# Optimization experiments

Hardware: AMD Instinct MI355X
Metric: run time of the kernel (lower is better)

Reference implementation:

```python
import jax, jax.numpy as jnp
import numpy as np
from jax import lax

B, L, E = 16, 100, 128
NQ, NC, DL = 1000, 100, 100
NODE, PATH, MAXC = 5000, 5000, 128


def setup_inputs() -> dict:
    key = jax.random.key(0)
    ks = jax.random.split(key, 40)
    rn = lambda k, *s: jax.random.normal(k, s, jnp.float32) * 0.02
    inp = {}
    inp['code'] = jax.random.randint(ks[0], (B, L, NQ * 2 + MAXC * 3), 0, NODE, jnp.int32)
    inp['q'] = jax.random.randint(ks[1], (B, L), 0, NQ, jnp.int32)
    inp['c'] = jax.random.randint(ks[2], (B, L), 0, NC, jnp.int32)
    inp['sd'] = jax.random.randint(ks[3], (B, L), 0, DL, jnp.int32)
    inp['qd'] = jax.random.randint(ks[4], (B, L), 0, DL, jnp.int32)
    inp['a'] = jax.random.randint(ks[5], (B, L), 0, NQ * 2, jnp.int32)
    inp['qshft'] = jax.random.randint(ks[6], (B, L), 0, NQ, jnp.int32)
    inp['cshft'] = jax.random.randint(ks[7], (B, L), 0, NC, jnp.int32)
    inp['sdshft'] = jax.random.randint(ks[8], (B, L), 0, DL, jnp.int32)
    inp['qdshft'] = jax.random.randint(ks[9], (B, L), 0, DL, jnp.int32)
    # embedding tables (padding rows zeroed, matching torch padding_idx)
    inp['embed_nodes'] = rn(ks[10], NODE + 2, E)
    inp['embed_paths'] = rn(ks[11], PATH + 2, E)
    inp['q_tab'] = rn(ks[12], NQ + 1, E).at[NQ].set(0.0)
    inp['c_tab'] = rn(ks[13], NC + 1, E).at[NC].set(0.0)
    inp['sd_tab'] = rn(ks[14], DL + 100, E).at[0].set(0.0)
    inp['qd_tab'] = rn(ks[15], DL + 100, E).at[0].set(0.0)
    inp['a_tab'] = rn(ks[16], NQ * 2 + 2, E).at[2].set(0.0)
    inp['knowledge'] = rn(ks[17], 1, E)
    # linear weights stored [in, out] so y = x @ W + b
    inp['Wpt'] = rn(ks[18], 3 * E, 3 * E); inp['bpt'] = rn(ks[19], 3 * E)
    inp['Wat'] = rn(ks[20], 3 * E, 1);     inp['bat'] = rn(ks[21], 1)
    inp['Wqa'] = rn(ks[22], 4 * E, E);     inp['bqa'] = rn(ks[23], E)
    inp['W1'] = rn(ks[24], 4 * E, E);      inp['b1'] = rn(ks[25], E)
    inp['W2'] = rn(ks[26], E, E);          inp['b2'] = rn(ks[27], E)
    inp['W3'] = rn(ks[28], E, E);          inp['b3'] = rn(ks[29], E)
    inp['W4'] = rn(ks[30], 2 * E, E);      inp['b4'] = rn(ks[31], E)
    inp['W5'] = rn(ks[32], 2 * E, E);      inp['b5'] = rn(ks[33], E)
    inp['W6'] = rn(ks[34], 4 * E, E);      inp['b6'] = rn(ks[35], E)
    inp['Wf'] = rn(ks[36], E, 10);         inp['bf'] = rn(ks[37], 10)
    return inp


def reference(code, q, c, sd, qd, a, qshft, cshft, sdshft, qdshft,
              embed_nodes, embed_paths, q_tab, c_tab, sd_tab, qd_tab, a_tab,
              knowledge, Wpt, bpt, Wat, bat, Wqa, bqa, W1, b1, W2, b2, W3, b3,
              W4, b4, W5, b5, W6, b6, Wf, bf):
    Bq, Lq = q.shape
    # ---- code2vec attention over AST paths ----
    c2v = code[:, :, NQ * 2:].reshape(Bq, Lq, MAXC, 3)
    full = jnp.concatenate([embed_nodes[c2v[..., 0]],
                            embed_nodes[c2v[..., 2]],
                            embed_paths[c2v[..., 1]]], axis=-1)  # [B,L,MAXC,3E]
    tr = jnp.tanh(full @ Wpt + bpt)
    ctx = tr @ Wat + bat                      # [B,L,MAXC,1]
    attn = jax.nn.softmax(ctx, axis=1)        # softmax over seq dim (dim=1), as in source
    code_vec = jnp.sum(full * attn, axis=2)   # [B,L,3E]
    # ---- embeddings + input projections ----
    a_e = a_tab[a]
    acode = jnp.concatenate([a_e, code_vec], axis=-1) @ Wqa + bqa   # [B,L,E]
    inp = jnp.concatenate([q_tab[q], c_tab[c], sd_tab[sd], qd_tab[qd]], axis=-1) @ W1 + b1
    sd_e = sd_tab[sd]
    qd_e = qd_tab[qd]
    # ---- sequential SDF/PKA/KSU recurrence ----
    k0 = jnp.tile(knowledge, (Bq, 1))  # [B,E]

    def step(k, ts):
        inp_t, a_t, sd_t, qd_t = ts
        qq = inp_t - k
        sdf = jax.nn.sigmoid(qq @ W2 + b2) * jnp.tanh(qq @ W3 + b3)
        x = jnp.concatenate([sdf, a_t], axis=-1)
        pka = jax.nn.sigmoid(x @ W4 + b4) * jnp.tanh(x @ W5 + b5)
        ins = jnp.concatenate([k, a_t, sd_t, qd_t], axis=-1)
        g = jax.nn.sigmoid(ins @ W6 + b6)
        k_new = g * k + (1.0 - g) * pka
        return k_new, k_new @ Wf + bf

    xs = (inp.transpose(1, 0, 2), acode.transpose(1, 0, 2),
          sd_e.transpose(1, 0, 2), qd_e.transpose(1, 0, 2))
    _, logits = lax.scan(step, k0, xs)        # [L,B,10]
    return jax.nn.sigmoid(logits.transpose(1, 0, 2))  # [B,L,10]
```

## Files before the change

### kernel.cpp

```cpp
#include <hip/hip_runtime.h>
#include <hip/hip_bf16.h>

#define B_   16
#define L_   100
#define E_   128
#define NQ_  1000
#define MAXC_ 128
#define CODE_STRIDE (NQ_*2 + MAXC_*3)
#define CODE_OFF    (NQ_*2)

typedef short bf16x8 __attribute__((ext_vector_type(8)));
typedef float f32x4  __attribute__((ext_vector_type(4)));

__device__ __forceinline__ unsigned short f2b(float f) {
    unsigned u = __float_as_uint(f);
    unsigned r = (u + 0x7fffu + ((u >> 16) & 1u)) >> 16;
    return (unsigned short)r;
}
__device__ __forceinline__ unsigned cvt2(float lo, float hi) {
    unsigned r;
    asm("v_cvt_pk_bf16_f32 %0, %1, %2" : "=v"(r) : "v"(lo), "v"(hi));
    return r;
}
__device__ __forceinline__ float fsig(float x) {
    return __builtin_amdgcn_rcpf(1.0f + __builtin_amdgcn_exp2f(-1.44269504f * x));
}
__device__ __forceinline__ float ftanh(float x) {
    return 1.0f - 2.0f * __builtin_amdgcn_rcpf(1.0f + __builtin_amdgcn_exp2f(2.88539008f * x));
}
__device__ __forceinline__ void ldsbar() {
    asm volatile("s_waitcnt lgkmcnt(0)" ::: "memory");
    __builtin_amdgcn_s_barrier();
}
__device__ __forceinline__ void vmbar() {
    asm volatile("s_waitcnt vmcnt(0) lgkmcnt(0)" ::: "memory");
    __builtin_amdgcn_s_barrier();
}
__device__ __forceinline__ void gll16(const void* g, void* l) {
    __builtin_amdgcn_global_load_lds(
        (const __attribute__((address_space(1))) unsigned int*)g,
        (__attribute__((address_space(3))) unsigned int*)l, 16, 0, 0);
}

#define P0 576
#define P1 (P0+2501)
#define P2 (P1+2501)
#define P3 (P2+192)
#define P4 (P3+128)
#define P5 (P4+8)
#define P6 (P5+512)
#define P7 (P6+256)
#define P8 (P7+192)

__global__ void k_prep(const float* __restrict__ Wpt, const float* __restrict__ en,
                       const float* __restrict__ ep,
                       const float* __restrict__ W2, const float* __restrict__ W3,
                       const float* __restrict__ W4, const float* __restrict__ W5,
                       const float* __restrict__ W6, const float* __restrict__ Wf,
                       const float* __restrict__ Wqa, const float* __restrict__ W1,
                       unsigned short* __restrict__ wptT, unsigned short* __restrict__ enb,
                       unsigned short* __restrict__ epb, unsigned short* __restrict__ bt1,
                       unsigned short* __restrict__ bt2, unsigned short* __restrict__ btf,
                       unsigned short* __restrict__ bW1, unsigned short* __restrict__ bW2,
                       unsigned short* __restrict__ bW6)
{
    int blk = blockIdx.x;
    if (blk < P0) {
        int i = blk * 256 + threadIdx.x;
        if (i < 384*384) {
            int e = i & 7, G = i >> 3;
            int l15g = G & 15, rest = G >> 4;
            int l4g = rest & 3, rest2 = rest >> 2;
            int ksg = rest2 % 12, tile = rest2 / 12;
            int n = tile*16 + l15g, k = ksg*32 + l4g*8 + e;
            wptT[i] = f2b(Wpt[k*384 + n]);
        }
    } else if (blk < P1) {
        int i = (blk - P0) * 256 + threadIdx.x;
        if (i < 5002*128) enb[i] = f2b(en[i]);
    } else if (blk < P2) {
        int i = (blk - P1) * 256 + threadIdx.x;
        if (i < 5002*128) epb[i] = f2b(ep[i]);
    } else if (blk < P3) {
        int i = (blk - P2) * 256 + threadIdx.x;
        int n = i >> 7, k = i & 127;
        float v = (n < 128) ? W2[k*128 + n] : (n < 256) ? W3[k*128 + (n-128)]
                                                        : W6[k*128 + (n-256)];
        bt1[i] = f2b(v);
    } else if (blk < P4) {
        int i = (blk - P3) * 256 + threadIdx.x;
        int n = i >> 7, k = i & 127;
        float v = (n < 128) ? W4[k*128 + n] : W5[k*128 + (n-128)];
        bt2[i] = f2b(v);
    } else if (blk < P5) {
        int i = (blk - P4) * 256 + threadIdx.x;
        int n = i >> 7, k = i & 127;
        btf[i] = f2b(n < 10 ? Wf[k*10 + n] : 0.0f);
    } else if (blk < P6) {
        int i = (blk - P5) * 256 + threadIdx.x;
        int n = i >> 9, k = i & 511;
        float v = (n < 128) ? Wqa[k*128 + n] : W1[k*128 + (n-128)];
        bW1[i] = f2b(v);
    } else if (blk < P7) {
        int i = (blk - P6) * 256 + threadIdx.x;
        int n = i >> 7, k = i & 127;
        float v = (n < 128) ? W2[k*128 + n]
                : (n < 256) ? W3[k*128 + (n-128)]
                : (n < 384) ? W4[(128 + k)*128 + (n-256)]
                            : W5[(128 + k)*128 + (n-384)];
        bW2[i] = f2b(v);
    } else {
        int i = (blk - P7) * 256 + threadIdx.x;
        if (i < 128*384) {
            int n = i / 384, k = i % 384;
            bW6[i] = f2b(W6[(128 + k)*128 + n]);
        }
    }
}

__global__ __launch_bounds__(256, 3) void k_ctx(const int* __restrict__ code,
    const unsigned short* __restrict__ enb, const unsigned short* __restrict__ epb,
    const unsigned short* __restrict__ wptT, const float* __restrict__ bpt,
    const float* __restrict__ wat, const float* __restrict__ bat,
    float* __restrict__ ctx)
{
    __shared__ __align__(16) unsigned short Bs[2][12288];
    __shared__ float bw[768];
    const int tid = threadIdx.x, wv = tid >> 6, lane = tid & 63;
    const int l15 = lane & 15, l4 = lane >> 4;
    const int rowg0 = blockIdx.x * 128;

    for (int idx = tid; idx < 768; idx += 256)
        bw[idx] = (idx < 384) ? bpt[idx] : wat[idx - 384];

    bf16x8 af[2][12];
    #pragma unroll
    for (int h = 0; h < 2; ++h) {
        int rowg = rowg0 + h * 64 + wv * 16 + l15;
        int m = rowg & 127, bl = rowg >> 7;
        const int* cp = code + (size_t)bl * CODE_STRIDE + CODE_OFF + m * 3;
        int i0 = cp[0], i1 = cp[1], i2 = cp[2];
        #pragma unroll
        for (int ks = 0; ks < 12; ++ks) {
            int seg = ks >> 2;
            int idx = (seg == 0) ? i0 : (seg == 1 ? i2 : i1);
            const unsigned short* tab = (seg == 2) ? epb : enb;
            af[h][ks] = *(const bf16x8*)(tab + (size_t)idx * 128 + (ks & 3) * 32 + l4 * 8);
        }
    }

    {
        const unsigned short* src = wptT;
        #pragma unroll
        for (int i = 0; i < 6; ++i) {
            int jj = wv * 6 + i;
            gll16(src + jj * 512 + lane * 8, &Bs[0][jj * 512]);
        }
    }

    float cr[2][4] = {{0.f,0.f,0.f,0.f},{0.f,0.f,0.f,0.f}};
    const float bat0 = bat[0];

    for (int nc = 0; nc < 12; ++nc) {
        vmbar();
        if (nc < 11) {
            const unsigned short* src = wptT + (size_t)(nc + 1) * 12288;
            #pragma unroll
            for (int i = 0; i < 6; ++i) {
                int jj = wv * 6 + i;
                gll16(src + jj * 512 + lane * 8, &Bs[(nc + 1) & 1][jj * 512]);
            }
        }
        const char* bb0 = (const char*)&Bs[nc & 1][0] + l15 * 16;
        const char* bb1 = bb0 + 12288;
        f32x4 acc00 = {0.f,0.f,0.f,0.f}, acc01 = {0.f,0.f,0.f,0.f};
        f32x4 acc10 = {0.f,0.f,0.f,0.f}, acc11 = {0.f,0.f,0.f,0.f};
        #pragma unroll
        for (int ks = 0; ks < 12; ++ks) {
            int go = (ks * 4 + l4) * 256;
            bf16x8 b0 = *(const bf16x8*)(bb0 + go);
            bf16x8 b1 = *(const bf16x8*)(bb1 + go);
            acc00 = __builtin_amdgcn_mfma_f32_16x16x32_bf16(af[0][ks], b0, acc00, 0, 0, 0);
            acc01 = __builtin_amdgcn_mfma_f32_16x16x32_bf16(af[0][ks], b1, acc01, 0, 0, 0);
            acc10 = __builtin_amdgcn_mfma_f32_16x16x32_bf16(af[1][ks], b0, acc10, 0, 0, 0);
            acc11 = __builtin_amdgcn_mfma_f32_16x16x32_bf16(af[1][ks], b1, acc11, 0, 0, 0);
        }
        int ng0 = nc * 32 + l15, ng1 = ng0 + 16;
        float bv0 = bw[ng0], wa0 = bw[384 + ng0];
        float bv1 = bw[ng1], wa1 = bw[384 + ng1];
        #pragma unroll
        for (int r = 0; r < 4; ++r) {
            cr[0][r] += ftanh(acc00[r] + bv0) * wa0 + ftanh(acc01[r] + bv1) * wa1;
            cr[1][r] += ftanh(acc10[r] + bv0) * wa0 + ftanh(acc11[r] + bv1) * wa1;
        }
    }

    #pragma unroll
    for (int h = 0; h < 2; ++h)
        #pragma unroll
        for (int r = 0; r < 4; ++r) {
            float v = cr[h][r];
            v += __shfl_xor(v, 1); v += __shfl_xor(v, 2);
            v += __shfl_xor(v, 4); v += __shfl_xor(v, 8);
            cr[h][r] = v;
        }
    if (l15 == 0) {
        #pragma unroll
        for (int h = 0; h < 2; ++h) {
            int rbase = rowg0 + h * 64 + wv * 16 + l4 * 4;
            #pragma unroll
            for (int r = 0; r < 4; ++r) ctx[rbase + r] = cr[h][r] + bat0;
        }
    }
}

__global__ void k_softmax(const float* __restrict__ ctx, float* __restrict__ attn)
{
    int t = blockIdx.x * 256 + threadIdx.x;
    if (t >= B_ * MAXC_) return;
    int b = t >> 7, m = t & 127;
    const float* p = ctx + (size_t)b * L_ * MAXC_ + m;
    float mx = -1e30f;
    for (int l = 0; l < L_; ++l) mx = fmaxf(mx, p[l * MAXC_]);
    float s = 0.f;
    for (int l = 0; l < L_; ++l) s += __expf(p[l * MAXC_] - mx);
    float inv = 1.0f / s;
    float* o = attn + (size_t)b * L_ * MAXC_ + m;
    for (int l = 0; l < L_; ++l) o[l * MAXC_] = __expf(p[l * MAXC_] - mx) * inv;
}

__global__ __launch_bounds__(192) void k_codevec(const int* __restrict__ code,
    const float* __restrict__ attn, const unsigned short* __restrict__ enb,
    const unsigned short* __restrict__ epb, float* __restrict__ cv)
{
    int bl = blockIdx.x;
    int t = threadIdx.x;
    int seg = t >> 6, tc = t & 63;
    const int* cp = code + (size_t)bl * CODE_STRIDE + CODE_OFF;
    const float* ap = attn + (size_t)bl * MAXC_;
    const unsigned short* tab = (seg == 2) ? epb : enb;
    const int sidx = (seg == 0) ? 0 : (seg == 1) ? 2 : 1;
    float ax = 0.f, ay = 0.f;
    #pragma unroll 8
    for (int m = 0; m < MAXC_; ++m) {
        float w = ap[m];
        int idx = cp[m * 3 + sidx];
        unsigned u = *((const unsigned*)(tab + (size_t)idx * 128) + tc);
        ax += w * __uint_as_float(u << 16);
        ay += w * __uint_as_float(u & 0xffff0000u);
    }
    float2 o; o.x = ax; o.y = ay;
    *(float2*)(cv + (size_t)bl * 384 + seg * 128 + tc * 2) = o;
}

__global__ __launch_bounds__(256) void k_fuse(
    const int* __restrict__ a, const int* __restrict__ q, const int* __restrict__ c,
    const int* __restrict__ sd, const int* __restrict__ qd,
    const float* __restrict__ a_tab, const float* __restrict__ q_tab,
    const float* __restrict__ c_tab, const float* __restrict__ sd_tab,
    const float* __restrict__ qd_tab, const float* __restrict__ cv,
    const unsigned short* __restrict__ bW1, const unsigned short* __restrict__ bW2,
    const unsigned short* __restrict__ bW6,
    const float* __restrict__ bqa, const float* __restrict__ b1,
    const float* __restrict__ b2, const float* __restrict__ b3,
    const float* __restrict__ b4, const float* __restrict__ b5,
    const float* __restrict__ b6,
    float4* __restrict__ preQ, float* __restrict__ pre6)
{
    __shared__ __align__(16) unsigned short X[16 * 1024];
    __shared__ __align__(16) unsigned short Y[16 * 256];
    const int tid = threadIdx.x, wv = tid >> 6, lane = tid & 63;
    const int l15 = lane & 15, l4 = lane >> 4;
    const int row0 = blockIdx.x * 16;

    #pragma unroll
    for (int it = 0; it < 16; ++it) {
        int idx = tid + it * 256;
        int r = idx >> 8, col = (idx & 255) * 4;
        int row = row0 + r;
        const float* src;
        if (col < 128)       src = a_tab + (size_t)a[row] * 128 + col;
        else if (col < 512)  src = cv + (size_t)row * 384 + (col - 128);
        else if (col < 640)  src = q_tab + (size_t)q[row] * 128 + (col - 512);
        else if (col < 768)  src = c_tab + (size_t)c[row] * 128 + (col - 640);
        else if (col < 896)  src = sd_tab + (size_t)sd[row] * 128 + (col - 768);
        else                 src = qd_tab + (size_t)qd[row] * 128 + (col - 896);
        float4 v = *(const float4*)src;
        unsigned u0 = cvt2(v.x, v.y), u1 = cvt2(v.z, v.w);
        int byte = r * 2048 + ((((col >> 3)) ^ (r & 7)) << 4) + ((col & 4) << 1);
        *(unsigned*)((char*)X + byte) = u0;
        *(unsigned*)((char*)X + byte + 4) = u1;
    }
    ldsbar();

    {
        bf16x8 ak[16];
        int kbase = (wv < 2) ? 0 : 512;
        #pragma unroll
        for (int ks = 0; ks < 16; ++ks) {
            int col = kbase + ks * 32 + l4 * 8;
            ak[ks] = *(const bf16x8*)((const char*)X + l15 * 2048 + (((col >> 3) ^ (l15 & 7)) << 4));
        }
        int nbase = wv * 64;
        f32x4 acc[4] = {{0,0,0,0},{0,0,0,0},{0,0,0,0},{0,0,0,0}};
        #pragma unroll
        for (int i = 0; i < 4; ++i) {
            const unsigned short* bp = bW1 + (size_t)(nbase + i * 16 + l15) * 512 + l4 * 8;
            #pragma unroll
            for (int ks = 0; ks < 16; ++ks) {
                bf16x8 bfr = *(const bf16x8*)(bp + ks * 32);
                acc[i] = __builtin_amdgcn_mfma_f32_16x16x32_bf16(ak[ks], bfr, acc[i], 0, 0, 0);
            }
        }
        #pragma unroll
        for (int i = 0; i < 4; ++i) {
            int cc = nbase + i * 16 + l15;
            float bias = (cc < 128) ? bqa[cc] : b1[cc - 128];
            #pragma unroll
            for (int rr = 0; rr < 4; ++rr) {
                int row = l4 * 4 + rr;
                int byte = row * 512 + (((cc >> 3) ^ (row & 7)) << 4) + (cc & 7) * 2;
                *(unsigned short*)((char*)Y + byte) = f2b(acc[i][rr] + bias);
            }
        }
    }
    ldsbar();

    bf16x8 zi[4], za[4], zs[4], zq[4];
    #pragma unroll
    for (int ks = 0; ks < 4; ++ks) {
        int ci = 128 + ks * 32 + l4 * 8;
        zi[ks] = *(const bf16x8*)((const char*)Y + l15 * 512 + (((ci >> 3) ^ (l15 & 7)) << 4));
        int ca = ks * 32 + l4 * 8;
        za[ks] = *(const bf16x8*)((const char*)Y + l15 * 512 + (((ca >> 3) ^ (l15 & 7)) << 4));
        int cs = 768 + ks * 32 + l4 * 8;
        zs[ks] = *(const bf16x8*)((const char*)X + l15 * 2048 + (((cs >> 3) ^ (l15 & 7)) << 4));
        int cq = 896 + ks * 32 + l4 * 8;
        zq[ks] = *(const bf16x8*)((const char*)X + l15 * 2048 + (((cq >> 3) ^ (l15 & 7)) << 4));
    }
    f32x4 A2[2] = {{0,0,0,0},{0,0,0,0}}, A3[2] = {{0,0,0,0},{0,0,0,0}};
    f32x4 A4[2] = {{0,0,0,0},{0,0,0,0}}, A5[2] = {{0,0,0,0},{0,0,0,0}};
    f32x4 A6[2] = {{0,0,0,0},{0,0,0,0}};
    #pragma unroll
    for (int tt = 0; tt < 2; ++tt) {
        int n = wv * 32 + tt * 16 + l15;
        const unsigned short* p2 = bW2 + (size_t)(      n) * 128 + l4 * 8;
        const unsigned short* p3 = bW2 + (size_t)(128 + n) * 128 + l4 * 8;
        const unsigned short* p4 = bW2 + (size_t)(256 + n) * 128 + l4 * 8;
        const unsigned short* p5 = bW2 + (size_t)(384 + n) * 128 + l4 * 8;
        const unsigned short* p6 = bW6 + (size_t)n * 384 + l4 * 8;
        #pragma unroll
        for (int ks = 0; ks < 4; ++ks) {
            A2[tt] = __builtin_amdgcn_mfma_f32_16x16x32_bf16(zi[ks], *(const bf16x8*)(p2 + ks*32), A2[tt], 0, 0, 0);
            A3[tt] = __builtin_amdgcn_mfma_f32_16x16x32_bf16(zi[ks], *(const bf16x8*)(p3 + ks*32), A3[tt], 0, 0, 0);
            A4[tt] = __builtin_amdgcn_mfma_f32_16x16x32_bf16(za[ks], *(const bf16x8*)(p4 + ks*32), A4[tt], 0, 0, 0);
            A5[tt] = __builtin_amdgcn_mfma_f32_16x16x32_bf16(za[ks], *(const bf16x8*)(p5 + ks*32), A5[tt], 0, 0, 0);
            A6[tt] = __builtin_amdgcn_mfma_f32_16x16x32_bf16(za[ks], *(const bf16x8*)(p6 + ks*32), A6[tt], 0, 0, 0);
        }
        #pragma unroll
        for (int ks = 0; ks < 4; ++ks)
            A6[tt] = __builtin_amdgcn_mfma_f32_16x16x32_bf16(zs[ks], *(const bf16x8*)(p6 + 256 + ks*32), A6[tt], 0, 0, 0);
        #pragma unroll
        for (int ks = 0; ks < 4; ++ks)
            A6[tt] = __builtin_amdgcn_mfma_f32_16x16x32_bf16(zq[ks], *(const bf16x8*)(p6 + 512 + ks*32), A6[tt], 0, 0, 0);
    }
    #pragma unroll
    for (int tt = 0; tt < 2; ++tt) {
        int n = wv * 32 + tt * 16 + l15;
        float c2 = b2[n], c3 = b3[n], c4 = b4[n], c5 = b5[n], c6 = b6[n];
        #pragma unroll
        for (int rr = 0; rr < 4; ++rr) {
            size_t row = (size_t)(row0 + l4 * 4 + rr);
            float4 o;
            o.x = A2[tt][rr] + c2; o.y = A3[tt][rr] + c3;
            o.z = A4[tt][rr] + c4; o.w = A5[tt][rr] + c5;
            preQ[row * 128 + n] = o;
            pre6[row * 128 + n] = A6[tt][rr] + c6;
        }
    }
}

__global__ __launch_bounds__(512) void k_recur(
    const unsigned short* __restrict__ bt1, const unsigned short* __restrict__ bt2,
    const float* __restrict__ knowledge, const float4* __restrict__ preQ,
    const float* __restrict__ pre6, unsigned short* __restrict__ khist)
{
    __shared__ __align__(16) unsigned short k_lds[16 * 128];
    __shared__ __align__(16) unsigned short s_lds[16 * 128];
    const int tid = threadIdx.x, wv = tid >> 6, lane = tid & 63;
    const int l15 = lane & 15, l4 = lane >> 4;
    const int j = wv * 16 + l15;

    bf16x8 w2f[4], w3f[4], w6f[4], w4f[4], w5f[4];
    #pragma unroll
    for (int ks = 0; ks < 4; ++ks) {
        w2f[ks] = *(const bf16x8*)(bt1 + (size_t)(      j) * 128 + ks * 32 + l4 * 8);
        w3f[ks] = *(const bf16x8*)(bt1 + (size_t)(128 + j) * 128 + ks * 32 + l4 * 8);
        w6f[ks] = *(const bf16x8*)(bt1 + (size_t)(256 + j) * 128 + ks * 32 + l4 * 8);
        w4f[ks] = *(const bf16x8*)(bt2 + (size_t)(      j) * 128 + ks * 32 + l4 * 8);
        w5f[ks] = *(const bf16x8*)(bt2 + (size_t)(128 + j) * 128 + ks * 32 + l4 * 8);
    }

    float kreg[4], gR[4];
    {
        float k0 = knowledge[j];
        unsigned short kb = f2b(k0);
        #pragma unroll
        for (int r = 0; r < 4; ++r) {
            kreg[r] = k0;
            int b = l4 * 4 + r;
            k_lds[b * 128 + (((j >> 3) ^ b) << 3) + (j & 7)] = kb;
        }
    }
    ldsbar();

    float4 pv[4]; float p6[4];
    #pragma unroll
    for (int r = 0; r < 4; ++r) {
        int b = l4 * 4 + r;
        size_t ix = (size_t)(b * L_) * 128 + j;
        pv[r] = preQ[ix]; p6[r] = pre6[ix];
    }

    for (int t = 0; t < L_; ++t) {
        float4 pvN[4]; float p6N[4];
        #pragma unroll
        for (int r = 0; r < 4; ++r) {
            int b = l4 * 4 + r;
            size_t ix = (size_t)(b * L_ + t + 1) * 128 + j;
            pvN[r] = preQ[ix]; p6N[r] = pre6[ix];
        }

        bf16x8 ak[4];
        {
            const unsigned short* kb = k_lds + l15 * 128;
            #pragma unroll
            for (int ks = 0; ks < 4; ++ks)
                ak[ks] = *(const bf16x8*)(kb + (((ks * 4 + l4) ^ l15) << 3));
        }
        f32x4 a2 = {0,0,0,0}, a3 = {0,0,0,0}, a6 = {0,0,0,0};
        #pragma unroll
        for (int ks = 0; ks < 4; ++ks) {
            a2 = __builtin_amdgcn_mfma_f32_16x16x32_bf16(ak[ks], w2f[ks], a2, 0, 0, 0);
            a3 = __builtin_amdgcn_mfma_f32_16x16x32_bf16(ak[ks], w3f[ks], a3, 0, 0, 0);
            a6 = __builtin_amdgcn_mfma_f32_16x16x32_bf16(ak[ks], w6f[ks], a6, 0, 0, 0);
        }
        #pragma unroll
        for (int r = 0; r < 4; ++r) {
            int b = l4 * 4 + r;
            float sdf = fsig(pv[r].x - a2[r]) * ftanh(pv[r].y - a3[r]);
            gR[r] = fsig(a6[r] + p6[r]);
            s_lds[b * 128 + (((j >> 3) ^ b) << 3) + (j & 7)] = f2b(sdf);
        }
        ldsbar();
        bf16x8 as[4];
        {
            const unsigned short* sb = s_lds + l15 * 128;
            #pragma unroll
            for (int ks = 0; ks < 4; ++ks)
                as[ks] = *(const bf16x8*)(sb + (((ks * 4 + l4) ^ l15) << 3));
        }
        f32x4 a4 = {0,0,0,0}, a5 = {0,0,0,0};
        #pragma unroll
        for (int ks = 0; ks < 4; ++ks) {
            a4 = __builtin_amdgcn_mfma_f32_16x16x32_bf16(as[ks], w4f[ks], a4, 0, 0, 0);
            a5 = __builtin_amdgcn_mfma_f32_16x16x32_bf16(as[ks], w5f[ks], a5, 0, 0, 0);
        }
        #pragma unroll
        for (int r = 0; r < 4; ++r) {
            int b = l4 * 4 + r;
            float pka = fsig(a4[r] + pv[r].z) * ftanh(a5[r] + pv[r].w);
            float kn = gR[r] * kreg[r] + (1.0f - gR[r]) * pka;
            kreg[r] = kn;
            unsigned short kb2 = f2b(kn);
            k_lds[b * 128 + (((j >> 3) ^ b) << 3) + (j & 7)] = kb2;
            khist[(size_t)(b * L_ + t) * 128 + j] = kb2;
        }
        #pragma unroll
        for (int r = 0; r < 4; ++r) { pv[r] = pvN[r]; p6[r] = p6N[r]; }
        ldsbar();
    }
}

__global__ __launch_bounds__(256) void k_logits(const unsigned short* __restrict__ khist,
    const unsigned short* __restrict__ btf, const float* __restrict__ bfv,
    float* __restrict__ out)
{
    int wv = threadIdx.x >> 6, lane = threadIdx.x & 63;
    int l15 = lane & 15, l4 = lane >> 4;
    int R0 = (blockIdx.x * 4 + wv) * 16;
    bf16x8 wbf[4], akr[4];
    #pragma unroll
    for (int ks = 0; ks < 4; ++ks)
        wbf[ks] = *(const bf16x8*)(btf + (size_t)l15 * 128 + ks * 32 + l4 * 8);
    const unsigned short* kb = khist + (size_t)(R0 + l15) * 128;
    #pragma unroll
    for (int ks = 0; ks < 4; ++ks)
        akr[ks] = *(const bf16x8*)(kb + ks * 32 + l4 * 8);
    f32x4 af = {0.f, 0.f, 0.f, 0.f};
    #pragma unroll
    for (int ks = 0; ks < 4; ++ks)
        af = __builtin_amdgcn_mfma_f32_16x16x32_bf16(akr[ks], wbf[ks], af, 0, 0, 0);
    if (l15 < 10) {
        float bb = bfv[l15];
        #pragma unroll
        for (int r = 0; r < 4; ++r)
            out[(size_t)(R0 + l4 * 4 + r) * 10 + l15] = fsig(af[r] + bb);
    }
}

extern "C" void kernel_launch(void* const* d_in, const int* in_sizes, int n_in,
                              void* d_out, int out_size, void* d_ws, size_t ws_size,
                              hipStream_t stream)
{
    const int*   code  = (const int*)d_in[0];
    const int*   q     = (const int*)d_in[1];
    const int*   c     = (const int*)d_in[2];
    const int*   sd    = (const int*)d_in[3];
    const int*   qd    = (const int*)d_in[4];
    const int*   a     = (const int*)d_in[5];
    const float* en    = (const float*)d_in[10];
    const float* ep    = (const float*)d_in[11];
    const float* q_tab = (const float*)d_in[12];
    const float* c_tab = (const float*)d_in[13];
    const float* sd_tab= (const float*)d_in[14];
    const float* qd_tab= (const float*)d_in[15];
    const float* a_tab = (const float*)d_in[16];
    const float* know  = (const float*)d_in[17];
    const float* Wpt   = (const float*)d_in[18];
    const float* bpt   = (const float*)d_in[19];
    const float* Wat   = (const float*)d_in[20];
    const float* bat   = (const float*)d_in[21];
    const float* Wqa   = (const float*)d_in[22];
    const float* bqa   = (const float*)d_in[23];
    const float* W1    = (const float*)d_in[24];
    const float* b1    = (const float*)d_in[25];
    const float* W2    = (const float*)d_in[26];
    const float* b2    = (const float*)d_in[27];
    const float* W3    = (const float*)d_in[28];
    const float* b3    = (const float*)d_in[29];
    const float* W4    = (const float*)d_in[30];
    const float* b4    = (const float*)d_in[31];
    const float* W5    = (const float*)d_in[32];
    const float* b5    = (const float*)d_in[33];
    const float* W6    = (const float*)d_in[34];
    const float* b6    = (const float*)d_in[35];
    const float* Wf    = (const float*)d_in[36];
    const float* bf_   = (const float*)d_in[37];

    char* ws = (char*)d_ws;
    size_t off = 0;
    auto alloc = [&](size_t n) { size_t r = off; off += (n + 255) & ~(size_t)255; return r; };
    unsigned short* wptT = (unsigned short*)(ws + alloc(384 * 384 * 2));
    unsigned short* enb  = (unsigned short*)(ws + alloc(5002 * 128 * 2));
    unsigned short* epb  = (unsigned short*)(ws + alloc(5002 * 128 * 2));
    unsigned short* bt1  = (unsigned short*)(ws + alloc(384 * 128 * 2));
    unsigned short* bt2  = (unsigned short*)(ws + alloc(256 * 128 * 2));
    unsigned short* btf  = (unsigned short*)(ws + alloc(16 * 128 * 2));
    unsigned short* bW1  = (unsigned short*)(ws + alloc(256 * 512 * 2));
    unsigned short* bW2  = (unsigned short*)(ws + alloc(512 * 128 * 2));
    unsigned short* bW6  = (unsigned short*)(ws + alloc(128 * 384 * 2));
    float* ctx   = (float*)(ws + alloc((size_t)B_ * L_ * MAXC_ * 4));
    float* attn  = (float*)(ws + alloc((size_t)B_ * L_ * MAXC_ * 4));
    float* cv    = (float*)(ws + alloc((size_t)B_ * L_ * 384 * 4));
    float4* preQ = (float4*)(ws + alloc(((size_t)B_ * L_ * 128 + 128) * 16));
    float* pre6  = (float*)(ws + alloc(((size_t)B_ * L_ * 128 + 128) * 4));
    unsigned short* khist = (unsigned short*)(ws + alloc((size_t)B_ * L_ * 128 * 2));
    float* outf  = (float*)d_out;

    k_prep<<<P8, 256, 0, stream>>>(Wpt, en, ep, W2, W3, W4, W5, W6, Wf,
                                   Wqa, W1,
                                   wptT, enb, epb, bt1, bt2, btf,
                                   bW1, bW2, bW6);
    k_ctx<<<1600, 256, 0, stream>>>(code, enb, epb, wptT, bpt, Wat, bat, ctx);
    k_softmax<<<8, 256, 0, stream>>>(ctx, attn);
    k_codevec<<<1600, 192, 0, stream>>>(code, attn, enb, epb, cv);
    k_fuse<<<100, 256, 0, stream>>>(a, q, c, sd, qd, a_tab, q_tab, c_tab, sd_tab,
                                    qd_tab, cv, bW1, bW2, bW6, bqa, b1,
                                    b2, b3, b4, b5, b6, preQ, pre6);
    k_recur<<<1, 512, 0, stream>>>(bt1, bt2, know, preQ, pre6, khist);
    k_logits<<<25, 256, 0, stream>>>(khist, btf, bf_, outf);
}
```

Before: 288.0 us.

## Fuse softmax exp and sum into ctx GEMM and enlarge ctx row tiles

Removes the separate softmax kernel. The ctx kernel now writes exp of the attention score and atomically accumulates per-(batch,slot) sums. The codevec kernel normalizes by that sum in shared memory. The ctx kernel also processes 192 rows per block with a 3x3 MFMA tile over 48-column chunks, for more B-tile reuse at lower occupancy. The max-subtraction is dropped, which risks overflow for large scores, and atomics add contention.

```diff
diff --git a/kernel.cpp b/kernel.cpp
--- a/kernel.cpp
+++ b/kernel.cpp
@@ -8,6 +8,7 @@
 #define MAXC_ 128
 #define CODE_STRIDE (NQ_*2 + MAXC_*3)
 #define CODE_OFF    (NQ_*2)
+#define NROWS (B_*L_*MAXC_)
 
 typedef short bf16x8 __attribute__((ext_vector_type(8)));
 typedef float f32x4  __attribute__((ext_vector_type(4)));
@@ -51,6 +52,7 @@
 #define P6 (P5+512)
 #define P7 (P6+256)
 #define P8 (P7+192)
+#define P9 (P8+8)
 
 __global__ void k_prep(const float* __restrict__ Wpt, const float* __restrict__ en,
                        const float* __restrict__ ep,
@@ -62,7 +64,7 @@
                        unsigned short* __restrict__ epb, unsigned short* __restrict__ bt1,
                        unsigned short* __restrict__ bt2, unsigned short* __restrict__ btf,
                        unsigned short* __restrict__ bW1, unsigned short* __restrict__ bW2,
-                       unsigned short* __restrict__ bW6)
+                       unsigned short* __restrict__ bW6, float* __restrict__ ssum)
 {
     int blk = blockIdx.x;
     if (blk < P0) {
@@ -109,35 +111,39 @@
                 : (n < 384) ? W4[(128 + k)*128 + (n-256)]
                             : W5[(128 + k)*128 + (n-384)];
         bW2[i] = f2b(v);
-    } else {
+    } else if (blk < P8) {
         int i = (blk - P7) * 256 + threadIdx.x;
         if (i < 128*384) {
             int n = i / 384, k = i % 384;
             bW6[i] = f2b(W6[(128 + k)*128 + n]);
         }
-    }
-}
-
-__global__ __launch_bounds__(256, 3) void k_ctx(const int* __restrict__ code,
+    } else {
+        int i = (blk - P8) * 256 + threadIdx.x;
+        if (i < B_ * MAXC_) ssum[i] = 0.0f;
+    }
+}
+
+__global__ __launch_bounds__(256, 2) void k_ctx(const int* __restrict__ code,
     const unsigned short* __restrict__ enb, const unsigned short* __restrict__ epb,
     const unsigned short* __restrict__ wptT, const float* __restrict__ bpt,
     const float* __restrict__ wat, const float* __restrict__ bat,
-    float* __restrict__ ctx)
-{
-    __shared__ __align__(16) unsigned short Bs[2][12288];
+    float* __restrict__ ectx, float* __restrict__ ssum)
+{
+    __shared__ __align__(16) unsigned short Bs[2][18432];
     __shared__ float bw[768];
     const int tid = threadIdx.x, wv = tid >> 6, lane = tid & 63;
     const int l15 = lane & 15, l4 = lane >> 4;
-    const int rowg0 = blockIdx.x * 128;
+    const int rowg0 = blockIdx.x * 192;
 
     for (int idx = tid; idx < 768; idx += 256)
         bw[idx] = (idx < 384) ? bpt[idx] : wat[idx - 384];
 
-    bf16x8 af[2][12];
-    #pragma unroll
-    for (int h = 0; h < 2; ++h) {
+    bf16x8 af[3][12];
+    #pragma unroll
+    for (int h = 0; h < 3; ++h) {
         int rowg = rowg0 + h * 64 + wv * 16 + l15;
-        int m = rowg & 127, bl = rowg >> 7;
+        int rowc = (rowg < NROWS) ? rowg : (NROWS - 1);
+        int m = rowc & 127, bl = rowc >> 7;
         const int* cp = code + (size_t)bl * CODE_STRIDE + CODE_OFF + m * 3;
         int i0 = cp[0], i1 = cp[1], i2 = cp[2];
         #pragma unroll
@@ -152,51 +158,56 @@
     {
         const unsigned short* src = wptT;
         #pragma unroll
-        for (int i = 0; i < 6; ++i) {
-            int jj = wv * 6 + i;
-            gll16(src + jj * 512 + lane * 8, &Bs[0][jj * 512]);
-        }
-    }
-
-    float cr[2][4] = {{0.f,0.f,0.f,0.f},{0.f,0.f,0.f,0.f}};
+        for (int i = 0; i < 9; ++i) {
+            int g0 = wv * 64 + i * 256;
+            gll16(src + (size_t)g0 * 8 + lane * 8, &Bs[0][g0 * 8]);
+        }
+    }
+
+    float cr[3][4] = {{0,0,0,0},{0,0,0,0},{0,0,0,0}};
     const float bat0 = bat[0];
 
-    for (int nc = 0; nc < 12; ++nc) {
+    for (int nc = 0; nc < 8; ++nc) {
         vmbar();
-        if (nc < 11) {
-            const unsigned short* src = wptT + (size_t)(nc + 1) * 12288;
-            #pragma unroll
-            for (int i = 0; i < 6; ++i) {
-                int jj = wv * 6 + i;
-                gll16(src + jj * 512 + lane * 8, &Bs[(nc + 1) & 1][jj * 512]);
+        if (nc < 7) {
+            const unsigned short* src = wptT + (size_t)(nc + 1) * 18432;
+            #pragma unroll
+            for (int i = 0; i < 9; ++i) {
+                int g0 = wv * 64 + i * 256;
+                gll16(src + (size_t)g0 * 8 + lane * 8, &Bs[(nc + 1) & 1][g0 * 8]);
             }
         }
-        const char* bb0 = (const char*)&Bs[nc & 1][0] + l15 * 16;
-        const char* bb1 = bb0 + 12288;
-        f32x4 acc00 = {0.f,0.f,0.f,0.f}, acc01 = {0.f,0.f,0.f,0.f};
-        f32x4 acc10 = {0.f,0.f,0.f,0.f}, acc11 = {0.f,0.f,0.f,0.f};
+        const char* bb = (const char*)&Bs[nc & 1][0] + l15 * 16;
+        f32x4 acc[3][3] = {{{0,0,0,0},{0,0,0,0},{0,0,0,0}},
+                           {{0,0,0,0},{0,0,0,0},{0,0,0,0}},
+                           {{0,0,0,0},{0,0,0,0},{0,0,0,0}}};
         #pragma unroll
         for (int ks = 0; ks < 12; ++ks) {
             int go = (ks * 4 + l4) * 256;
-            bf16x8 b0 = *(const bf16x8*)(bb0 + go);
-            bf16x8 b1 = *(const bf16x8*)(bb1 + go);
-            acc00 = __builtin_amdgcn_mfma_f32_16x16x32_bf16(af[0][ks], b0, acc00, 0, 0, 0);
-            acc01 = __builtin_amdgcn_mfma_f32_16x16x32_bf16(af[0][ks], b1, acc01, 0, 0, 0);
-            acc10 = __builtin_amdgcn_mfma_f32_16x16x32_bf16(af[1][ks], b0, acc10, 0, 0, 0);
-            acc11 = __builtin_amdgcn_mfma_f32_16x16x32_bf16(af[1][ks], b1, acc11, 0, 0, 0);
-        }
-        int ng0 = nc * 32 + l15, ng1 = ng0 + 16;
-        float bv0 = bw[ng0], wa0 = bw[384 + ng0];
-        float bv1 = bw[ng1], wa1 = bw[384 + ng1];
-        #pragma unroll
-        for (int r = 0; r < 4; ++r) {
-            cr[0][r] += ftanh(acc00[r] + bv0) * wa0 + ftanh(acc01[r] + bv1) * wa1;
-            cr[1][r] += ftanh(acc10[r] + bv0) * wa0 + ftanh(acc11[r] + bv1) * wa1;
-        }
-    }
-
-    #pragma unroll
-    for (int h = 0; h < 2; ++h)
+            bf16x8 b0 = *(const bf16x8*)(bb + go);
+            bf16x8 b1 = *(const bf16x8*)(bb + 24576 + go);
+            bf16x8 b2 = *(const bf16x8*)(bb + 49152 + go);
+            #pragma unroll
+            for (int h = 0; h < 3; ++h) {
+                acc[h][0] = __builtin_amdgcn_mfma_f32_16x16x32_bf16(af[h][ks], b0, acc[h][0], 0, 0, 0);
+                acc[h][1] = __builtin_amdgcn_mfma_f32_16x16x32_bf16(af[h][ks], b1, acc[h][1], 0, 0, 0);
+                acc[h][2] = __builtin_amdgcn_mfma_f32_16x16x32_bf16(af[h][ks], b2, acc[h][2], 0, 0, 0);
+            }
+        }
+        #pragma unroll
+        for (int tt = 0; tt < 3; ++tt) {
+            int ng = nc * 48 + tt * 16 + l15;
+            float bv = bw[ng], wa = bw[384 + ng];
+            #pragma unroll
+            for (int h = 0; h < 3; ++h)
+                #pragma unroll
+                for (int r = 0; r < 4; ++r)
+                    cr[h][r] += ftanh(acc[h][tt][r] + bv) * wa;
+        }
+    }
+
+    #pragma unroll
+    for (int h = 0; h < 3; ++h)
         #pragma unroll
         for (int r = 0; r < 4; ++r) {
             float v = cr[h][r];
@@ -206,44 +217,43 @@
         }
     if (l15 == 0) {
         #pragma unroll
-        for (int h = 0; h < 2; ++h) {
+        for (int h = 0; h < 3; ++h) {
             int rbase = rowg0 + h * 64 + wv * 16 + l4 * 4;
             #pragma unroll
-            for (int r = 0; r < 4; ++r) ctx[rbase + r] = cr[h][r] + bat0;
-        }
-    }
-}
-
-__global__ void k_softmax(const float* __restrict__ ctx, float* __restrict__ attn)
-{
-    int t = blockIdx.x * 256 + threadIdx.x;
-    if (t >= B_ * MAXC_) return;
-    int b = t >> 7, m = t & 127;
-    const float* p = ctx + (size_t)b * L_ * MAXC_ + m;
-    float mx = -1e30f;
-    for (int l = 0; l < L_; ++l) mx = fmaxf(mx, p[l * MAXC_]);
-    float s = 0.f;
-    for (int l = 0; l < L_; ++l) s += __expf(p[l * MAXC_] - mx);
-    float inv = 1.0f / s;
-    float* o = attn + (size_t)b * L_ * MAXC_ + m;
-    for (int l = 0; l < L_; ++l) o[l * MAXC_] = __expf(p[l * MAXC_] - mx) * inv;
+            for (int r = 0; r < 4; ++r) {
+                int row = rbase + r;
+                if (row < NROWS) {
+                    float e = __builtin_amdgcn_exp2f((cr[h][r] + bat0) * 1.44269504f);
+                    ectx[row] = e;
+                    int bl = row >> 7, m = row & 127;
+                    atomicAdd(&ssum[(bl / 100) * 128 + m], e);
+                }
+            }
+        }
+    }
 }
 
 __global__ __launch_bounds__(192) void k_codevec(const int* __restrict__ code,
-    const float* __restrict__ attn, const unsigned short* __restrict__ enb,
-    const unsigned short* __restrict__ epb, float* __restrict__ cv)
-{
+    const float* __restrict__ ectx, const float* __restrict__ ssum,
+    const unsigned short* __restrict__ enb, const unsigned short* __restrict__ epb,
+    float* __restrict__ cv)
+{
+    __shared__ float sm[128];
     int bl = blockIdx.x;
     int t = threadIdx.x;
+    if (t < 128) {
+        sm[t] = ectx[(size_t)bl * MAXC_ + t]
+                * __builtin_amdgcn_rcpf(ssum[(bl / 100) * 128 + t]);
+    }
+    ldsbar();
     int seg = t >> 6, tc = t & 63;
     const int* cp = code + (size_t)bl * CODE_STRIDE + CODE_OFF;
-    const float* ap = attn + (size_t)bl * MAXC_;
     const unsigned short* tab = (seg == 2) ? epb : enb;
     const int sidx = (seg == 0) ? 0 : (seg == 1) ? 2 : 1;
     float ax = 0.f, ay = 0.f;
     #pragma unroll 8
     for (int m = 0; m < MAXC_; ++m) {
-        float w = ap[m];
+        float w = sm[m];
         int idx = cp[m * 3 + sidx];
         unsigned u = *((const unsigned*)(tab + (size_t)idx * 128) + tc);
         ax += w * __uint_as_float(u << 16);
@@ -560,21 +570,20 @@
     unsigned short* bW1  = (unsigned short*)(ws + alloc(256 * 512 * 2));
     unsigned short* bW2  = (unsigned short*)(ws + alloc(512 * 128 * 2));
     unsigned short* bW6  = (unsigned short*)(ws + alloc(128 * 384 * 2));
-    float* ctx   = (float*)(ws + alloc((size_t)B_ * L_ * MAXC_ * 4));
-    float* attn  = (float*)(ws + alloc((size_t)B_ * L_ * MAXC_ * 4));
+    float* ectx  = (float*)(ws + alloc((size_t)NROWS * 4));
+    float* ssum  = (float*)(ws + alloc((size_t)B_ * MAXC_ * 4));
     float* cv    = (float*)(ws + alloc((size_t)B_ * L_ * 384 * 4));
     float4* preQ = (float4*)(ws + alloc(((size_t)B_ * L_ * 128 + 128) * 16));
     float* pre6  = (float*)(ws + alloc(((size_t)B_ * L_ * 128 + 128) * 4));
     unsigned short* khist = (unsigned short*)(ws + alloc((size_t)B_ * L_ * 128 * 2));
     float* outf  = (float*)d_out;
 
-    k_prep<<<P8, 256, 0, stream>>>(Wpt, en, ep, W2, W3, W4, W5, W6, Wf,
+    k_prep<<<P9, 256, 0, stream>>>(Wpt, en, ep, W2, W3, W4, W5, W6, Wf,
                                    Wqa, W1,
                                    wptT, enb, epb, bt1, bt2, btf,
-                                   bW1, bW2, bW6);
-    k_ctx<<<1600, 256, 0, stream>>>(code, enb, epb, wptT, bpt, Wat, bat, ctx);
-    k_softmax<<<8, 256, 0, stream>>>(ctx, attn);
-    k_codevec<<<1600, 192, 0, stream>>>(code, attn, enb, epb, cv);
+                                   bW1, bW2, bW6, ssum);
+    k_ctx<<<1067, 256, 0, stream>>>(code, enb, epb, wptT, bpt, Wat, bat, ectx, ssum);
+    k_codevec<<<1600, 192, 0, stream>>>(code, ectx, ssum, enb, epb, cv);
     k_fuse<<<100, 256, 0, stream>>>(a, q, c, sd, qd, a_tab, q_tab, c_tab, sd_tab,
                                     qd_tab, cv, bW1, bW2, bW6, bqa, b1,
                                     b2, b3, b4, b5, b6, preQ, pre6);
```

Result: faster. 280.9 us (-2.5%).
